# Optimization experiments

Measured on AMD Instinct MI355X. Metric: run time of the kernel, lower is better.

## Reference

```python
import jax, jax.numpy as jnp
import numpy as np
import math

THR = 1.0
TAU_MEM = 20.0
TAU_TRACE = 20.0
DAMPENING = 0.3
DECAY_MEM = math.exp(-1.0 / TAU_MEM)
DECAY_TRACE = math.exp(-1.0 / TAU_TRACE)

@jax.custom_vjp
def spike(x):
    # Heaviside forward, triangular surrogate backward (SpikeFunction in repo)
    return (x > 0.0).astype(x.dtype)

def _spike_fwd(x):
    return spike(x), x

def _spike_bwd(x, g):
    return (g * DAMPENING * jnp.maximum(0.0, 1.0 - jnp.abs(x)),)

spike.defvjp(_spike_fwd, _spike_bwd)

def setup_inputs() -> dict:
    key = jax.random.key(0)
    k1, k2 = jax.random.split(key)
    B, T, I, H = 32, 1000, 256, 512
    x = jax.random.normal(k1, (B, T, I), dtype=jnp.float32)
    # xavier_uniform with gain sqrt(2)
    limit = math.sqrt(2.0) * math.sqrt(6.0 / (H + I))
    W = jax.random.uniform(k2, (H, I), dtype=jnp.float32, minval=-limit, maxval=limit)
    return {"x": x, "W": W}

def reference(x, W):
    B, T, _ = x.shape
    H = W.shape[0]
    # input currents for all timesteps at once: [B,T,H] -> scan over T
    i = jnp.einsum('bti,hi->bth', x, W)
    i_t = jnp.moveaxis(i, 1, 0)  # [T,B,H]

    v0 = jnp.zeros((B, H), x.dtype)
    z0 = jnp.zeros((B, H), x.dtype)
    tr0 = jnp.zeros((B, H), x.dtype)

    def step(carry, inp):
        v, z, trace = carry
        # LIF: multiplicative reset with detached spike
        v = DECAY_MEM * v * (1.0 - jax.lax.stop_gradient(z)) + (1.0 - DECAY_MEM) * inp
        z_new = spike((v - THR) / THR)
        trace = DECAY_TRACE * trace + (1.0 - DECAY_TRACE) * z_new  # exp_convolve
        return (v, z_new, trace), (z_new, trace)

    (v, z, trace), (out_seq, trace_seq) = jax.lax.scan(step, (v0, z0, tr0), i_t)
    out_seq = jnp.moveaxis(out_seq, 0, 1)    # [B,T,H]
    trace_seq = jnp.moveaxis(trace_seq, 0, 1)
    return out_seq, trace_seq
```

## Files before the change

### kernel.cpp

```cpp
#include <hip/hip_runtime.h>
#include <hip/hip_bf16.h>
#include <cstddef>

#define Bb 32
#define Tt 1000
#define Ii 256
#define Hh 512
#define CHK 192
#define NCHK 6

typedef __attribute__((ext_vector_type(8))) short short8;
typedef __attribute__((ext_vector_type(4))) float f32x4;

__device__ __forceinline__ unsigned short f2bfu(float f) {
  return __builtin_bit_cast(unsigned short, __float2bfloat16(f));
}

template <int NP>
__device__ __forceinline__ void scan_run(const unsigned int* cw,
                                         float* zp, float* tp,
                                         float& v, bool& zb, float& tr) {
  const float dm = 0.9512294245007140f, om = 0.0487705754992860f;
  unsigned int ring[8];
#pragma unroll
  for (int j = 0; j < 8; ++j)
    if (j < NP) ring[j] = cw[j];

  auto step = [&](unsigned int bits16, int t) {
    const float cur = __builtin_bit_cast(float, bits16 << 16);
    const float omc = om * cur;
    const float w = fmaf(v, dm, omc);
    v = zb ? omc : w;
    zb = v > 1.0f;
    tr = fmaf(tr, dm, zb ? om : 0.0f);
    __builtin_nontemporal_store(zb ? 1.0f : 0.0f, zp + (size_t)t * Hh);
    __builtin_nontemporal_store(tr, tp + (size_t)t * Hh);
  };

  int g = 0;
  for (; g + 8 <= NP; g += 8) {
#pragma unroll
    for (int j = 0; j < 8; ++j) {
      const unsigned int c2 = ring[j];
      if (g + j + 8 < NP) ring[j] = cw[g + j + 8];
      step(c2 & 0xffffu, 2 * (g + j));
      step(c2 >> 16, 2 * (g + j) + 1);
    }
  }
#pragma unroll
  for (int j = 0; j < 8; ++j) {
    if (j < (NP & 7)) {
      const unsigned int c2 = ring[j];
      step(c2 & 0xffffu, 2 * (g + j));
      step(c2 >> 16, 2 * (g + j) + 1);
    }
  }
}

__global__ __launch_bounds__(256, 1) void lif_fused(const float* __restrict__ X,
                                                    const float* __restrict__ W,
                                                    float* __restrict__ Z,
                                                    float* __restrict__ TR) {
  __shared__ short Ws[64 * 256];
  __shared__ short cc[2][64 * 194];

  const int tid = threadIdx.x;
  const int ht = blockIdx.x;
  const int b = blockIdx.y;
  const int lane = tid & 63;
  const int wid = tid >> 6;
  const int fl = lane & 15, fj = lane >> 4;

  {
    const int h = tid >> 2;
    const int j = tid & 3;
    const float* wg = W + (size_t)(ht * 64 + h) * Ii;
#pragma unroll
    for (int q = 0; q < 8; ++q) {
      const int slot = j * 8 + q;
      f32x4 w0 = *(const f32x4*)(wg + slot * 8);
      f32x4 w1 = *(const f32x4*)(wg + slot * 8 + 4);
      short8 wv;
#pragma unroll
      for (int e = 0; e < 4; ++e) {
        wv[e] = (short)f2bfu(w0[e]);
        wv[4 + e] = (short)f2bfu(w1[e]);
      }
      *(short8*)(Ws + h * 256 + ((slot ^ (h & 7)) << 3)) = wv;
    }
  }
  __syncthreads();

  auto gemm_chunk = [&](int c, short* ccb) {
    const int ts = (wid - 1) * 64;
    const int t0 = c * CHK + ts;
    f32x4 acc[4][4];
#pragma unroll
    for (int i = 0; i < 4; ++i)
#pragma unroll
      for (int j = 0; j < 4; ++j) acc[i][j] = (f32x4)0.0f;

    const float* xb[4];
#pragma unroll
    for (int mi = 0; mi < 4; ++mi) {
      int row = t0 + mi * 16 + fl;
      row = (row < Tt) ? row : (Tt - 1);
      xb[mi] = X + ((size_t)b * Tt + row) * Ii + (fj << 3);
    }

#define LOADA(dst, s)                                                   \
  {                                                                     \
    _Pragma("unroll") for (int mi = 0; mi < 4; ++mi) {                  \
      dst[mi][0] = *(const f32x4*)(xb[mi] + (s) * 32);                  \
      dst[mi][1] = *(const f32x4*)(xb[mi] + (s) * 32 + 4);              \
    }                                                                   \
  }
#define KSTEP(src, s)                                                   \
  {                                                                     \
    short8 af[4];                                                       \
    _Pragma("unroll") for (int mi = 0; mi < 4; ++mi) {                  \
      _Pragma("unroll") for (int e = 0; e < 4; ++e) {                   \
        af[mi][e] = (short)f2bfu(src[mi][0][e]);                        \
        af[mi][4 + e] = (short)f2bfu(src[mi][1][e]);                    \
      }                                                                 \
    }                                                                   \
    _Pragma("unroll") for (int nj = 0; nj < 4; ++nj) {                  \
      const int h0 = nj * 16 + fl;                                      \
      const int slot = (s) * 4 + fj;                                    \
      short8 bfr = *(const short8*)(Ws + h0 * 256 +                     \
                                    ((slot ^ (h0 & 7)) << 3));          \
      _Pragma("unroll") for (int mi = 0; mi < 4; ++mi)                  \
        acc[mi][nj] = __builtin_amdgcn_mfma_f32_16x16x32_bf16(          \
            af[mi], bfr, acc[mi][nj], 0, 0, 0);                         \
    }                                                                   \
  }

    f32x4 a0[4][2], a1[4][2];
    LOADA(a0, 0);
    LOADA(a1, 1);
#pragma unroll
    for (int sp = 0; sp < 4; ++sp) {
      KSTEP(a0, 2 * sp);
      if (sp < 3) LOADA(a0, 2 * sp + 2);
      KSTEP(a1, 2 * sp + 1);
      if (sp < 3) LOADA(a1, 2 * sp + 3);
    }
#undef LOADA
#undef KSTEP

#pragma unroll
    for (int nj = 0; nj < 4; ++nj) {
      const int h = nj * 16 + fl;
#pragma unroll
      for (int mi = 0; mi < 4; ++mi) {
        const int r = ts + mi * 16 + fj * 4;
#pragma unroll
        for (int qp = 0; qp < 2; ++qp) {
          const unsigned int pk =
              ((unsigned int)f2bfu(acc[mi][nj][2 * qp + 1]) << 16) |
              f2bfu(acc[mi][nj][2 * qp]);
          *(unsigned int*)(ccb + h * 194 + r + 2 * qp) = pk;
        }
      }
    }
  };

  float v = 0.0f, tr = 0.0f;
  bool zb = false;

  if (wid != 0) gemm_chunk(0, cc[0]);
  __syncthreads();

  for (int c = 0; c < NCHK; ++c) {
    if (wid == 0) {
      const unsigned int* cw = (const unsigned int*)(cc[c & 1] + lane * 194);
      float* zp = Z + ((size_t)b * Tt + c * CHK) * Hh + ht * 64 + lane;
      float* tp = TR + ((size_t)b * Tt + c * CHK) * Hh + ht * 64 + lane;
      if (c < NCHK - 1)
        scan_run<96>(cw, zp, tp, v, zb, tr);
      else
        scan_run<20>(cw, zp, tp, v, zb, tr);
    } else if (c + 1 < NCHK) {
      gemm_chunk(c + 1, cc[(c + 1) & 1]);
    }
    __syncthreads();
  }
}

extern "C" void kernel_launch(void* const* d_in, const int* in_sizes, int n_in,
                              void* d_out, int out_size, void* d_ws, size_t ws_size,
                              hipStream_t stream) {
  const float* x = (const float*)d_in[0];
  const float* W = (const float*)d_in[1];
  float* out = (float*)d_out;
  float* zout = out;
  float* trout = out + (size_t)Bb * Tt * Hh;

  dim3 grid(8, 32), block(256);
  hipLaunchKernelGGL(lif_fused, grid, block, 0, stream, x, W, zout, trout);
}
```

Measured before the change: 200.8 us.

## Pre-convert X to bf16 and stage chunks into LDS via async global_load_lds

Measured after the change: 185.2 us. -7.8%, faster.

```diff
diff --git a/kernel.cpp b/kernel.cpp
--- a/kernel.cpp
+++ b/kernel.cpp
@@ -6,8 +6,6 @@
 #define Tt 1000
 #define Ii 256
 #define Hh 512
-#define CHK 192
-#define NCHK 6
 
 typedef __attribute__((ext_vector_type(8))) short short8;
 typedef __attribute__((ext_vector_type(4))) float f32x4;
@@ -57,6 +55,153 @@
   }
 }
 
+__global__ __launch_bounds__(256) void cvt_x(const float* __restrict__ X,
+                                             short* __restrict__ XBF) {
+  const int gt = blockIdx.x * 256 + threadIdx.x;
+  const int row = gt >> 6, j = gt & 63;
+  f32x4 xv = *(const f32x4*)(X + (size_t)row * Ii + j * 4);
+  uint2 o;
+  o.x = ((unsigned)f2bfu(xv[1]) << 16) | f2bfu(xv[0]);
+  o.y = ((unsigned)f2bfu(xv[3]) << 16) | f2bfu(xv[2]);
+  *(uint2*)(XBF + (size_t)row * Ii + j * 4) = o;
+}
+
+#define CHK2 96
+#define NCHK2 11
+
+__global__ __launch_bounds__(256, 1) void lif_fused2(const short* __restrict__ XBF,
+                                                     const float* __restrict__ Wf,
+                                                     float* __restrict__ Z,
+                                                     float* __restrict__ TR) {
+  __shared__ short Ab[2][CHK2 * 256];
+  __shared__ short cc[2][64 * 98];
+
+  const int tid = threadIdx.x;
+  const int ht = blockIdx.x;
+  const int b = blockIdx.y;
+  const int lane = tid & 63;
+  const int wid = tid >> 6;
+  const int fl = lane & 15, fj = lane >> 4;
+  const int ts = (wid - 1) * 32;
+
+  short8 wfrag[8][4];
+  if (wid) {
+#pragma unroll
+    for (int s = 0; s < 8; ++s)
+#pragma unroll
+      for (int nj = 0; nj < 4; ++nj) {
+        const float* wp = Wf + (size_t)(ht * 64 + nj * 16 + fl) * Ii + s * 32 + fj * 8;
+        f32x4 w0 = *(const f32x4*)wp, w1 = *(const f32x4*)(wp + 4);
+        short8 vv;
+#pragma unroll
+        for (int e = 0; e < 4; ++e) {
+          vv[e] = (short)f2bfu(w0[e]);
+          vv[4 + e] = (short)f2bfu(w1[e]);
+        }
+        wfrag[s][nj] = vv;
+      }
+  }
+
+  const short* xb = XBF + (size_t)b * Tt * Ii;
+
+  auto stage = [&](int c, int buf) {
+#pragma unroll
+    for (int i = 0; i < 16; ++i) {
+      const int tloc = ts + 2 * i + (lane >> 5);
+      const int sp = lane & 31;
+      const int ks = sp ^ (tloc & 7);
+      int tg = c * CHK2 + tloc;
+      tg = tg < Tt ? tg : (Tt - 1);
+      const short* src = xb + (size_t)tg * Ii + ks * 8;
+      __builtin_amdgcn_global_load_lds(
+          (const __attribute__((address_space(1))) void*)src,
+          (__attribute__((address_space(3))) void*)(&Ab[buf][(ts + 2 * i) * 256]),
+          16, 0, 0);
+    }
+  };
+
+  auto gemm_chunk = [&](int buf, short* ccb) {
+    f32x4 acc[2][4];
+#pragma unroll
+    for (int mt = 0; mt < 2; ++mt)
+#pragma unroll
+      for (int nj = 0; nj < 4; ++nj) acc[mt][nj] = (f32x4)0.0f;
+
+    const short* Abase = &Ab[buf][0];
+#pragma unroll
+    for (int s = 0; s < 8; ++s) {
+      short8 af[2];
+#pragma unroll
+      for (int mt = 0; mt < 2; ++mt) {
+        const int tloc = ts + mt * 16 + fl;
+        const int slot = (4 * s + fj) ^ (tloc & 7);
+        af[mt] = *(const short8*)(Abase + tloc * 256 + slot * 8);
+      }
+#pragma unroll
+      for (int mt = 0; mt < 2; ++mt)
+#pragma unroll
+        for (int nj = 0; nj < 4; ++nj)
+          acc[mt][nj] = __builtin_amdgcn_mfma_f32_16x16x32_bf16(
+              af[mt], wfrag[s][nj], acc[mt][nj], 0, 0, 0);
+    }
+#pragma unroll
+    for (int mt = 0; mt < 2; ++mt)
+#pragma unroll
+      for (int nj = 0; nj < 4; ++nj) {
+        const int h = nj * 16 + fl;
+        const int r = ts + mt * 16 + fj * 4;
+#pragma unroll
+        for (int qp = 0; qp < 2; ++qp) {
+          const unsigned int pk =
+              ((unsigned)f2bfu(acc[mt][nj][2 * qp + 1]) << 16) |
+              f2bfu(acc[mt][nj][2 * qp]);
+          *(unsigned int*)(ccb + h * 98 + r + 2 * qp) = pk;
+        }
+      }
+  };
+
+  if (wid) {
+    stage(0, 0);
+    stage(1, 1);
+    asm volatile("s_waitcnt vmcnt(16)" ::: "memory");
+    gemm_chunk(0, &cc[0][0]);
+    asm volatile("s_waitcnt lgkmcnt(0)" ::: "memory");
+  }
+  __builtin_amdgcn_s_barrier();
+  asm volatile("" ::: "memory");
+
+  float v = 0.0f, tr = 0.0f;
+  bool zb = false;
+
+  for (int c = 0; c < NCHK2; ++c) {
+    if (wid == 0) {
+      const unsigned int* cw = (const unsigned int*)(&cc[c & 1][0] + lane * 98);
+      float* zp = Z + ((size_t)b * Tt + c * CHK2) * Hh + ht * 64 + lane;
+      float* tp = TR + ((size_t)b * Tt + c * CHK2) * Hh + ht * 64 + lane;
+      if (c < NCHK2 - 1)
+        scan_run<48>(cw, zp, tp, v, zb, tr);
+      else
+        scan_run<20>(cw, zp, tp, v, zb, tr);
+    } else {
+      if (c + 2 < NCHK2) {
+        stage(c + 2, c & 1);
+        asm volatile("s_waitcnt vmcnt(16)" ::: "memory");
+      } else if (c + 1 < NCHK2) {
+        asm volatile("s_waitcnt vmcnt(0)" ::: "memory");
+      }
+      if (c + 1 < NCHK2) {
+        gemm_chunk((c + 1) & 1, &cc[(c + 1) & 1][0]);
+        asm volatile("s_waitcnt lgkmcnt(0)" ::: "memory");
+      }
+    }
+    __builtin_amdgcn_s_barrier();
+    asm volatile("" ::: "memory");
+  }
+}
+
+#define CHK 192
+#define NCHK 6
+
 __global__ __launch_bounds__(256, 1) void lif_fused(const float* __restrict__ X,
                                                     const float* __restrict__ W,
                                                     float* __restrict__ Z,
@@ -100,19 +245,19 @@
 #pragma unroll
       for (int j = 0; j < 4; ++j) acc[i][j] = (f32x4)0.0f;
 
-    const float* xb[4];
+    const float* xbp[4];
 #pragma unroll
     for (int mi = 0; mi < 4; ++mi) {
       int row = t0 + mi * 16 + fl;
       row = (row < Tt) ? row : (Tt - 1);
-      xb[mi] = X + ((size_t)b * Tt + row) * Ii + (fj << 3);
+      xbp[mi] = X + ((size_t)b * Tt + row) * Ii + (fj << 3);
     }
 
 #define LOADA(dst, s)                                                   \
   {                                                                     \
     _Pragma("unroll") for (int mi = 0; mi < 4; ++mi) {                  \
-      dst[mi][0] = *(const f32x4*)(xb[mi] + (s) * 32);                  \
-      dst[mi][1] = *(const f32x4*)(xb[mi] + (s) * 32 + 4);              \
+      dst[mi][0] = *(const f32x4*)(xbp[mi] + (s) * 32);                 \
+      dst[mi][1] = *(const f32x4*)(xbp[mi] + (s) * 32 + 4);             \
     }                                                                   \
   }
 #define KSTEP(src, s)                                                   \
@@ -196,6 +341,14 @@
   float* zout = out;
   float* trout = out + (size_t)Bb * Tt * Hh;
 
-  dim3 grid(8, 32), block(256);
-  hipLaunchKernelGGL(lif_fused, grid, block, 0, stream, x, W, zout, trout);
-}
+  const size_t xbf_bytes = (size_t)Bb * Tt * Ii * sizeof(short);
+  if (ws_size >= xbf_bytes) {
+    short* xbf = (short*)d_ws;
+    hipLaunchKernelGGL(cvt_x, dim3(8000), dim3(256), 0, stream, x, xbf);
+    hipLaunchKernelGGL(lif_fused2, dim3(8, 32), dim3(256), 0, stream,
+                       xbf, W, zout, trout);
+  } else {
+    hipLaunchKernelGGL(lif_fused, dim3(8, 32), dim3(256), 0, stream,
+                       x, W, zout, trout);
+  }
+}
```

## Rotate scan role across waves with smaller chunks and register-resident weights

Applied to the files above, without the earlier changes.

Result: slower. 212.1 us (+5.6%).

```diff
diff --git a/kernel.cpp b/kernel.cpp
--- a/kernel.cpp
+++ b/kernel.cpp
@@ -6,8 +6,8 @@
 #define Tt 1000
 #define Ii 256
 #define Hh 512
-#define CHK 192
-#define NCHK 6
+#define CHK 96
+#define NPH 11
 
 typedef __attribute__((ext_vector_type(8))) short short8;
 typedef __attribute__((ext_vector_type(4))) float f32x4;
@@ -57,12 +57,12 @@
   }
 }
 
-__global__ __launch_bounds__(256, 1) void lif_fused(const float* __restrict__ X,
-                                                    const float* __restrict__ W,
-                                                    float* __restrict__ Z,
-                                                    float* __restrict__ TR) {
-  __shared__ short Ws[64 * 256];
-  __shared__ short cc[2][64 * 194];
+__global__ __launch_bounds__(256, 1) void lif_fused3(const float* __restrict__ X,
+                                                     const float* __restrict__ Wf,
+                                                     float* __restrict__ Z,
+                                                     float* __restrict__ TR) {
+  __shared__ short cc[2][64 * 98];
+  __shared__ float vst[64], trst[64], zst[64];
 
   const int tid = threadIdx.x;
   const int ht = blockIdx.x;
@@ -71,117 +71,101 @@
   const int wid = tid >> 6;
   const int fl = lane & 15, fj = lane >> 4;
 
-  {
-    const int h = tid >> 2;
-    const int j = tid & 3;
-    const float* wg = W + (size_t)(ht * 64 + h) * Ii;
+  short8 wfrag[8][4];
 #pragma unroll
-    for (int q = 0; q < 8; ++q) {
-      const int slot = j * 8 + q;
-      f32x4 w0 = *(const f32x4*)(wg + slot * 8);
-      f32x4 w1 = *(const f32x4*)(wg + slot * 8 + 4);
-      short8 wv;
+  for (int s = 0; s < 8; ++s)
+#pragma unroll
+    for (int nj = 0; nj < 4; ++nj) {
+      const float* wp = Wf + (size_t)(ht * 64 + nj * 16 + fl) * Ii + s * 32 + fj * 8;
+      f32x4 w0 = *(const f32x4*)wp, w1 = *(const f32x4*)(wp + 4);
+      short8 vv;
 #pragma unroll
       for (int e = 0; e < 4; ++e) {
-        wv[e] = (short)f2bfu(w0[e]);
-        wv[4 + e] = (short)f2bfu(w1[e]);
+        vv[e] = (short)f2bfu(w0[e]);
+        vv[4 + e] = (short)f2bfu(w1[e]);
       }
-      *(short8*)(Ws + h * 256 + ((slot ^ (h & 7)) << 3)) = wv;
-    }
-  }
-  __syncthreads();
-
-  auto gemm_chunk = [&](int c, short* ccb) {
-    const int ts = (wid - 1) * 64;
-    const int t0 = c * CHK + ts;
-    f32x4 acc[4][4];
-#pragma unroll
-    for (int i = 0; i < 4; ++i)
-#pragma unroll
-      for (int j = 0; j < 4; ++j) acc[i][j] = (f32x4)0.0f;
-
-    const float* xb[4];
-#pragma unroll
-    for (int mi = 0; mi < 4; ++mi) {
-      int row = t0 + mi * 16 + fl;
-      row = (row < Tt) ? row : (Tt - 1);
-      xb[mi] = X + ((size_t)b * Tt + row) * Ii + (fj << 3);
+      wfrag[s][nj] = vv;
     }
 
-#define LOADA(dst, s)                                                   \
-  {                                                                     \
-    _Pragma("unroll") for (int mi = 0; mi < 4; ++mi) {                  \
-      dst[mi][0] = *(const f32x4*)(xb[mi] + (s) * 32);                  \
-      dst[mi][1] = *(const f32x4*)(xb[mi] + (s) * 32 + 4);              \
-    }                                                                   \
-  }
-#define KSTEP(src, s)                                                   \
-  {                                                                     \
-    short8 af[4];                                                       \
-    _Pragma("unroll") for (int mi = 0; mi < 4; ++mi) {                  \
-      _Pragma("unroll") for (int e = 0; e < 4; ++e) {                   \
-        af[mi][e] = (short)f2bfu(src[mi][0][e]);                        \
-        af[mi][4 + e] = (short)f2bfu(src[mi][1][e]);                    \
-      }                                                                 \
-    }                                                                   \
-    _Pragma("unroll") for (int nj = 0; nj < 4; ++nj) {                  \
-      const int h0 = nj * 16 + fl;                                      \
-      const int slot = (s) * 4 + fj;                                    \
-      short8 bfr = *(const short8*)(Ws + h0 * 256 +                     \
-                                    ((slot ^ (h0 & 7)) << 3));          \
-      _Pragma("unroll") for (int mi = 0; mi < 4; ++mi)                  \
-        acc[mi][nj] = __builtin_amdgcn_mfma_f32_16x16x32_bf16(          \
-            af[mi], bfr, acc[mi][nj], 0, 0, 0);                         \
-    }                                                                   \
-  }
+  const float* xb = X + (size_t)b * Tt * Ii;
 
-    f32x4 a0[4][2], a1[4][2];
-    LOADA(a0, 0);
-    LOADA(a1, 1);
+  auto gemm_chunk = [&](int c, int r, short* ccb) {
+    const int ts = r * 32;
+    f32x4 a[2][8][2];
 #pragma unroll
-    for (int sp = 0; sp < 4; ++sp) {
-      KSTEP(a0, 2 * sp);
-      if (sp < 3) LOADA(a0, 2 * sp + 2);
-      KSTEP(a1, 2 * sp + 1);
-      if (sp < 3) LOADA(a1, 2 * sp + 3);
+    for (int mt = 0; mt < 2; ++mt) {
+      int row = c * CHK + ts + mt * 16 + fl;
+      row = row < Tt ? row : (Tt - 1);
+      const float* bp = xb + (size_t)row * Ii + fj * 8;
+#pragma unroll
+      for (int s = 0; s < 8; ++s) {
+        a[mt][s][0] = *(const f32x4*)(bp + s * 32);
+        a[mt][s][1] = *(const f32x4*)(bp + s * 32 + 4);
+      }
     }
-#undef LOADA
-#undef KSTEP
+    f32x4 acc[2][4];
+#pragma unroll
+    for (int mt = 0; mt < 2; ++mt)
+#pragma unroll
+      for (int nj = 0; nj < 4; ++nj) acc[mt][nj] = (f32x4)0.0f;
 
 #pragma unroll
-    for (int nj = 0; nj < 4; ++nj) {
-      const int h = nj * 16 + fl;
+    for (int s = 0; s < 8; ++s) {
+      short8 af[2];
 #pragma unroll
-      for (int mi = 0; mi < 4; ++mi) {
-        const int r = ts + mi * 16 + fj * 4;
+      for (int mt = 0; mt < 2; ++mt)
+#pragma unroll
+        for (int e = 0; e < 4; ++e) {
+          af[mt][e] = (short)f2bfu(a[mt][s][0][e]);
+          af[mt][4 + e] = (short)f2bfu(a[mt][s][1][e]);
+        }
+#pragma unroll
+      for (int mt = 0; mt < 2; ++mt)
+#pragma unroll
+        for (int nj = 0; nj < 4; ++nj)
+          acc[mt][nj] = __builtin_amdgcn_mfma_f32_16x16x32_bf16(
+              af[mt], wfrag[s][nj], acc[mt][nj], 0, 0, 0);
+    }
+#pragma unroll
+    for (int mt = 0; mt < 2; ++mt)
+#pragma unroll
+      for (int nj = 0; nj < 4; ++nj) {
+        const int h = nj * 16 + fl;
+        const int rr = ts + mt * 16 + fj * 4;
 #pragma unroll
         for (int qp = 0; qp < 2; ++qp) {
           const unsigned int pk =
-              ((unsigned int)f2bfu(acc[mi][nj][2 * qp + 1]) << 16) |
-              f2bfu(acc[mi][nj][2 * qp]);
-          *(unsigned int*)(ccb + h * 194 + r + 2 * qp) = pk;
+              ((unsigned)f2bfu(acc[mt][nj][2 * qp + 1]) << 16) |
+              f2bfu(acc[mt][nj][2 * qp]);
+          *(unsigned int*)(ccb + h * 98 + rr + 2 * qp) = pk;
         }
       }
-    }
   };
 
-  float v = 0.0f, tr = 0.0f;
-  bool zb = false;
-
-  if (wid != 0) gemm_chunk(0, cc[0]);
+  if (wid) gemm_chunk(0, wid - 1, &cc[0][0]);
   __syncthreads();
 
-  for (int c = 0; c < NCHK; ++c) {
-    if (wid == 0) {
-      const unsigned int* cw = (const unsigned int*)(cc[c & 1] + lane * 194);
+  for (int c = 0; c < NPH; ++c) {
+    const int s = c & 3;
+    if (wid == s) {
+      float v, tr;
+      bool zb;
+      if (c == 0) {
+        v = 0.0f; tr = 0.0f; zb = false;
+      } else {
+        v = vst[lane]; tr = trst[lane]; zb = (zst[lane] != 0.0f);
+      }
+      const unsigned int* cw = (const unsigned int*)(&cc[c & 1][0] + lane * 98);
       float* zp = Z + ((size_t)b * Tt + c * CHK) * Hh + ht * 64 + lane;
       float* tp = TR + ((size_t)b * Tt + c * CHK) * Hh + ht * 64 + lane;
-      if (c < NCHK - 1)
-        scan_run<96>(cw, zp, tp, v, zb, tr);
+      if (c < NPH - 1)
+        scan_run<48>(cw, zp, tp, v, zb, tr);
       else
         scan_run<20>(cw, zp, tp, v, zb, tr);
-    } else if (c + 1 < NCHK) {
-      gemm_chunk(c + 1, cc[(c + 1) & 1]);
+      vst[lane] = v; trst[lane] = tr; zst[lane] = zb ? 1.0f : 0.0f;
+    } else if (c + 1 < NPH) {
+      const int r = (wid - s - 1) & 3;
+      gemm_chunk(c + 1, r, &cc[(c + 1) & 1][0]);
     }
     __syncthreads();
   }
@@ -196,6 +180,6 @@
   float* zout = out;
   float* trout = out + (size_t)Bb * Tt * Hh;
 
-  dim3 grid(8, 32), block(256);
-  hipLaunchKernelGGL(lif_fused, grid, block, 0, stream, x, W, zout, trout);
+  hipLaunchKernelGGL(lif_fused3, dim3(8, 32), dim3(256), 0, stream,
+                     x, W, zout, trout);
 }
```
